# Performance work log

Hardware: AMD Instinct MI355X
Metric: run time of the kernel (lower is better)

## Reference

```python
import jax, jax.numpy as jnp
import numpy as np

DIM = 256; HEADS = 8; DK = 64; DV = 64; FH = 32; FW = 32; B = 16
INK = HEADS * DK; INV = HEADS * DV; N = FH * FW
SCALE = DK ** -0.5; EPS = 1e-5


def _pos_indices():
    pos = np.stack(np.meshgrid(np.arange(FH), np.arange(FW), indexing='ij'), axis=-1).reshape(-1, 2)
    rel = np.abs(pos[:, None, :] - pos[None, :, :])  # [N,N,2]
    return jnp.asarray(rel[..., 0] * FW + rel[..., 1], jnp.int32)  # [N,N]


def _bn(x, g, b, m, v):
    # eval-mode BatchNorm2d over channel axis 1
    s = (g / jnp.sqrt(v + EPS))
    return x * s[None, :, None, None] + (b - m * s)[None, :, None, None]


def setup_inputs() -> dict:
    key = jax.random.key(0)
    ks = jax.random.split(key, 24)
    f32 = jnp.float32
    def bn_params(k, c):
        k1, k2, k3, k4 = jax.random.split(k, 4)
        return (jax.random.normal(k1, (c,), f32) * 0.1 + 1.0,
                jax.random.normal(k2, (c,), f32) * 0.1,
                jax.random.normal(k3, (c,), f32) * 0.1,
                jax.random.uniform(k4, (c,), f32) + 0.5)
    gq, bq, mq, vq = bn_params(ks[1], INK)
    gk, bk, mk, vk = bn_params(ks[3], INK)
    gv, bv, mv, vv = bn_params(ks[5], INV)
    go, bo, mo, vo = bn_params(ks[7], DIM)
    return {
        'x': jax.random.normal(ks[0], (B, DIM, FH, FW), f32),
        'wq': jax.random.normal(ks[2], (INK, DIM), f32) * (DIM ** -0.5),
        'gq': gq, 'bq': bq, 'mq': mq, 'vq': vq,
        'wk': jax.random.normal(ks[4], (INK, DIM), f32) * (DIM ** -0.5),
        'gk': gk, 'bk': bk, 'mk': mk, 'vk': vk,
        'wv': jax.random.normal(ks[6], (INV, DIM), f32) * (DIM ** -0.5),
        'gv': gv, 'bv': bv, 'mv': mv, 'vv': vv,
        'emb': jax.random.normal(ks[8], (N, HEADS), f32) * 0.02,
        'w_out': jax.random.normal(ks[9], (DIM, INV), f32) * (INV ** -0.5),
        'b_out': jax.random.normal(ks[10], (DIM,), f32) * 0.02,
        'go': go, 'bo': bo, 'mo': mo, 'vo': vo,
        'pos_indices': _pos_indices(),
    }


def reference(x, wq, gq, bq, mq, vq, wk, gk, bk, mk, vk, wv, gv, bv, mv, vv,
              emb, w_out, b_out, go, bo, mo, vo, pos_indices):
    b = x.shape[0]
    # 1x1 conv == channel matmul
    q = _bn(jnp.einsum('bchw,oc->bohw', x, wq), gq, bq, mq, vq)
    k = _bn(jnp.einsum('bchw,oc->bohw', x, wk), gk, bk, mk, vk)
    v = _bn(jnp.einsum('bchw,oc->bohw', x, wv), gv, bv, mv, vv)
    # 'b (h d) x y -> b h (x y) d'
    def split_heads(t, d):
        return t.reshape(b, HEADS, d, N).transpose(0, 1, 3, 2)
    q = split_heads(q, DK); k = split_heads(k, DK); v = split_heads(v, DV)
    dots = jnp.einsum('bhid,bhjd->bhij', q, k) * SCALE  # [b,h,N,N]
    bias = emb[pos_indices]                               # [N,N,h] gather
    dots = dots + jnp.transpose(bias, (2, 0, 1))[None] / SCALE
    attn = jax.nn.softmax(dots, axis=-1)
    out = jnp.einsum('bhij,bhjd->bhid', attn, v)
    out = out.transpose(0, 1, 3, 2).reshape(b, INV, FH, FW)  # 'b h (x y) d -> b (h d) x y'
    hs = out * jnp.clip(out + 3.0, 0.0, 6.0) / 6.0           # Hardswish
    y = jnp.einsum('bchw,oc->bohw', hs, w_out) + b_out[None, :, None, None]
    return _bn(y, go, bo, mo, vo)
```

## Files before the change

kernel.cpp:

```cpp
#include <hip/hip_runtime.h>

typedef __attribute__((ext_vector_type(4))) float f32x4;
typedef __attribute__((ext_vector_type(8))) _Float16 f16x8;
typedef __attribute__((ext_vector_type(4))) _Float16 f16x4;

static __device__ __forceinline__ f32x4 mfma16f(f16x8 a, f16x8 b, f32x4 c) {
    return __builtin_amdgcn_mfma_f32_16x16x32_f16(a, b, c, 0, 0, 0);
}

__global__ __launch_bounds__(256) void prep(
    const float* __restrict__ x,
    const float* __restrict__ s0, const float* __restrict__ s1,
    const float* __restrict__ s2, const float* __restrict__ s3,
    _Float16* __restrict__ d0h, _Float16* __restrict__ d0l,
    _Float16* __restrict__ d1h, _Float16* __restrict__ d1l,
    _Float16* __restrict__ d2h, _Float16* __restrict__ d2l,
    _Float16* __restrict__ d3h, _Float16* __restrict__ d3l,
    _Float16* __restrict__ xth, _Float16* __restrict__ xtl)
{
    __shared__ float lt[32][36];
    const int t = threadIdx.x;
    const int bid = blockIdx.x;
    if (bid < 2048) {
        const int seg = bid >> 9;
        const int i = (bid & 511) * 256 + t;
        const float* src = (seg == 0) ? s0 : (seg == 1) ? s1 : (seg == 2) ? s2 : s3;
        _Float16* dh = (seg == 0) ? d0h : (seg == 1) ? d1h : (seg == 2) ? d2h : d3h;
        _Float16* dl = (seg == 0) ? d0l : (seg == 1) ? d1l : (seg == 2) ? d2l : d3l;
        const float f = src[i];
        const _Float16 h = (_Float16)f;
        dh[i] = h;
        dl[i] = (_Float16)(f - (float)h);
    } else {
        const int bid2 = bid - 2048;
        const int c0 = (bid2 & 7) * 32, hw0 = ((bid2 >> 3) & 31) * 32, b = bid2 >> 8;
        {
            const int cl = t >> 3, hw4 = (t & 7) * 4;
            *(f32x4*)&lt[cl][hw4] = *(const f32x4*)&x[((size_t)(b * 256 + c0 + cl)) * 1024 + hw0 + hw4];
        }
        __syncthreads();
        {
            const int hwl = t >> 3, c4 = (t & 7) * 4;
            f16x4 hv, lv;
#pragma unroll
            for (int e = 0; e < 4; ++e) {
                const float f = lt[c4 + e][hwl];
                const _Float16 h = (_Float16)f;
                hv[e] = h;
                lv[e] = (_Float16)(f - (float)h);
            }
            const size_t off = ((size_t)(b * 1024 + hw0 + hwl)) * 256 + c0 + c4;
            *(f16x4*)(xth + off) = hv;
            *(f16x4*)(xtl + off) = lv;
        }
    }
}

__global__ __launch_bounds__(256) void qkv_mfma(
    const _Float16* __restrict__ xth, const _Float16* __restrict__ xtl,
    const _Float16* __restrict__ wqh, const _Float16* __restrict__ wql,
    const _Float16* __restrict__ wkh, const _Float16* __restrict__ wkl,
    const _Float16* __restrict__ wvh, const _Float16* __restrict__ wvl,
    const float* __restrict__ gq, const float* __restrict__ bq, const float* __restrict__ mq, const float* __restrict__ vq,
    const float* __restrict__ gk, const float* __restrict__ bk, const float* __restrict__ mk, const float* __restrict__ vk,
    const float* __restrict__ gv, const float* __restrict__ bv, const float* __restrict__ mv, const float* __restrict__ vv,
    _Float16* __restrict__ qh, _Float16* __restrict__ ql,
    _Float16* __restrict__ kh,
    _Float16* __restrict__ vt)
{
    __shared__ _Float16 Ah[128][72];
    __shared__ _Float16 Al[128][72];
    __shared__ float sc_l[128], tc_l[128];

    const int t = threadIdx.x;
    const int bn = blockIdx.x;
    const int m0 = blockIdx.y * 128;
    const int proj = bn >> 2;
    const int o0 = (bn & 3) * 128;
    const int bimg = m0 >> 10;
    const int nb = m0 & 1023;

    const _Float16* Wh = (proj == 0) ? wqh : (proj == 1) ? wkh : wvh;
    const _Float16* Wl = (proj == 0) ? wql : (proj == 1) ? wkl : wvl;
    const float* G  = (proj == 0) ? gq : (proj == 1) ? gk : gv;
    const float* Bt = (proj == 0) ? bq : (proj == 1) ? bk : bv;
    const float* Mn = (proj == 0) ? mq : (proj == 1) ? mk : mv;
    const float* Vr = (proj == 0) ? vq : (proj == 1) ? vk : vv;

    if (t < 128) {
        const int o = o0 + t;
        float s = G[o] / sqrtf(Vr[o] + 1e-5f);
        float tt = Bt[o] - Mn[o] * s;
        if (proj == 0) { s *= 0.125f; tt *= 0.125f; }
        sc_l[t] = s; tc_l[t] = tt;
    }

    const int wave = t >> 6, lane = t & 63;
    const int quad = lane >> 4, l16 = lane & 15;
    const int wm = (wave >> 1) * 64, wn = (wave & 1) * 64;

    f32x4 acc[4][4] = {};

    for (int c0 = 0; c0 < 256; c0 += 64) {
        __syncthreads();
        {
            int r = t >> 3;
            const int cs = (t & 7) * 8;
#pragma unroll
            for (int p = 0; p < 4; ++p, r += 32) {
                const size_t off = ((size_t)(bimg * 1024 + nb + r)) * 256 + c0 + cs;
                *(f16x8*)&Ah[r][cs] = *(const f16x8*)(xth + off);
                *(f16x8*)&Al[r][cs] = *(const f16x8*)(xtl + off);
            }
        }
        __syncthreads();
#pragma unroll
        for (int kk = 0; kk < 2; ++kk) {
            f16x8 ah[4], al[4], bh[4], bl[4];
#pragma unroll
            for (int mi = 0; mi < 4; ++mi) {
                ah[mi] = *(const f16x8*)&Ah[wm + mi * 16 + l16][kk * 32 + quad * 8];
                al[mi] = *(const f16x8*)&Al[wm + mi * 16 + l16][kk * 32 + quad * 8];
            }
#pragma unroll
            for (int nj = 0; nj < 4; ++nj) {
                const size_t off = ((size_t)(o0 + wn + nj * 16 + l16)) * 256 + c0 + kk * 32 + quad * 8;
                bh[nj] = *(const f16x8*)(Wh + off);
                if (proj < 2) bl[nj] = *(const f16x8*)(Wl + off);
            }
            if (proj < 2) {
#pragma unroll
                for (int nj = 0; nj < 4; ++nj)
#pragma unroll
                    for (int mi = 0; mi < 4; ++mi) {
                        acc[nj][mi] = mfma16f(bh[nj], ah[mi], acc[nj][mi]);
                        acc[nj][mi] = mfma16f(bh[nj], al[mi], acc[nj][mi]);
                        acc[nj][mi] = mfma16f(bl[nj], ah[mi], acc[nj][mi]);
                    }
            } else {
#pragma unroll
                for (int mi = 0; mi < 4; ++mi)
#pragma unroll
                    for (int nj = 0; nj < 4; ++nj) {
                        acc[mi][nj] = mfma16f(ah[mi], bh[nj], acc[mi][nj]);
                        acc[mi][nj] = mfma16f(al[mi], bh[nj], acc[mi][nj]);
                    }
            }
        }
    }

    if (proj < 2) {
        _Float16* Oh = (proj == 0) ? qh : kh;
#pragma unroll
        for (int nj = 0; nj < 4; ++nj) {
            const int olb = wn + nj * 16 + quad * 4;
            const int ob = o0 + olb;
            const int head = ob >> 6, d0 = ob & 63;
#pragma unroll
            for (int mi = 0; mi < 4; ++mi) {
                const int n = nb + wm + mi * 16 + l16;
                f16x4 hv, lv;
#pragma unroll
                for (int rr = 0; rr < 4; ++rr) {
                    const float val = acc[nj][mi][rr] * sc_l[olb + rr] + tc_l[olb + rr];
                    const _Float16 h = (_Float16)val;
                    hv[rr] = h;
                    lv[rr] = (_Float16)(val - (float)h);
                }
                const size_t off = (((size_t)(bimg * 8 + head)) * 1024 + n) * 64 + d0;
                *(f16x4*)(Oh + off) = hv;
                if (proj == 0) *(f16x4*)(ql + off) = lv;
            }
        }
    } else {
#pragma unroll
        for (int nj = 0; nj < 4; ++nj) {
            const int olb = wn + nj * 16 + l16;
            const int o = o0 + olb;
            const int head = o >> 6, d = o & 63;
            const float s = sc_l[olb], tt = tc_l[olb];
#pragma unroll
            for (int mi = 0; mi < 4; ++mi) {
                const int n0 = nb + wm + mi * 16 + quad * 4;
                f16x4 v4;
#pragma unroll
                for (int rr = 0; rr < 4; ++rr) v4[rr] = (_Float16)(acc[mi][nj][rr] * s + tt);
                *(f16x4*)(vt + (((size_t)(bimg * 8 + head)) * 64 + d) * 1024 + n0) = v4;
            }
        }
    }
}

__global__ __launch_bounds__(512, 4) void attn_mfma(
    const _Float16* __restrict__ qh, const _Float16* __restrict__ ql,
    const _Float16* __restrict__ kh,
    const _Float16* __restrict__ vt,
    const float* __restrict__ emb,
    _Float16* __restrict__ hsh)
{
    __shared__ float    emb_s[1024];
    __shared__ _Float16 kth[64][76];
    __shared__ _Float16 vts[64][76];

    const int t = threadIdx.x;
    const int bid = blockIdx.x;
    const int bh = bid & 127, qb = bid >> 7;
    const int b = bh >> 3, h = bh & 7;
    const int wave = t >> 6, lane = t & 63;
    const int quad = lane >> 4, l16 = lane & 15;
    const int q0 = qb * 128 + wave * 16;
    const float L2E = 1.44269504f;

    for (int i = t; i < 1024; i += 512) emb_s[i] = (8.0f * emb[i * 8 + h] - 12.0f) * L2E;

    const size_t base = (size_t)bh * 65536;

    f16x8 qfh[2], qfl[2];
#pragma unroll
    for (int kk = 0; kk < 2; ++kk) {
        const size_t off = base + (size_t)(q0 + l16) * 64 + kk * 32 + quad * 8;
        qfh[kk] = *(const f16x8*)(qh + off);
        qfl[kk] = *(const f16x8*)(ql + off);
    }

    const int ig0 = q0 + l16;
    const int xi = ig0 >> 5, yi = ig0 & 31;

    const int sr = t >> 3;
    const int scs = (t & 7) * 8;

    f16x8 pkh, pvv;
    pkh = *(const f16x8*)(kh + base + (size_t)sr * 64 + scs);
    pvv = *(const f16x8*)(vt + base + (size_t)sr * 1024 + scs);

    f32x4 ao[4] = {};
    float lsum = 0.0f;

    for (int jb = 0; jb < 16; ++jb) {
        __syncthreads();
        *(f16x8*)&kth[sr][scs] = pkh;
        *(f16x8*)&vts[sr][scs] = pvv;
        __syncthreads();
        if (jb < 15) {
            pkh = *(const f16x8*)(kh + base + (size_t)((jb + 1) * 64 + sr) * 64 + scs);
            pvv = *(const f16x8*)(vt + base + (size_t)sr * 1024 + (jb + 1) * 64 + scs);
        }

#pragma unroll
        for (int nj = 0; nj < 4; ++nj) {
            const f16x8 kf0 = *(const f16x8*)&kth[nj * 16 + l16][quad * 8];
            const f16x8 kf1 = *(const f16x8*)&kth[nj * 16 + l16][32 + quad * 8];

            f32x4 ss = {};
            __builtin_amdgcn_s_setprio(1);
            ss = mfma16f(kf0, qfh[0], ss);
            ss = mfma16f(kf0, qfl[0], ss);
            ss = mfma16f(kf1, qfh[1], ss);
            ss = mfma16f(kf1, qfl[1], ss);
            __builtin_amdgcn_s_setprio(0);

            const int xj = 2 * jb + (nj >> 1);
            const int yj0 = ((nj & 1) << 4) + quad * 4;
            const int dxo = abs(xi - xj) << 5;
            const int yq = yi - yj0;
            const float p0 = __builtin_amdgcn_exp2f(fmaf(ss[0], L2E, emb_s[dxo + abs(yq)]));
            const float p1 = __builtin_amdgcn_exp2f(fmaf(ss[1], L2E, emb_s[dxo + abs(yq - 1)]));
            const float p2 = __builtin_amdgcn_exp2f(fmaf(ss[2], L2E, emb_s[dxo + abs(yq - 2)]));
            const float p3 = __builtin_amdgcn_exp2f(fmaf(ss[3], L2E, emb_s[dxo + abs(yq - 3)]));
            lsum += (p0 + p1) + (p2 + p3);
            f16x4 pa;
            pa[0] = (_Float16)p0; pa[1] = (_Float16)p1;
            pa[2] = (_Float16)p2; pa[3] = (_Float16)p3;

            f16x4 vf[4];
#pragma unroll
            for (int dj = 0; dj < 4; ++dj)
                vf[dj] = *(const f16x4*)&vts[dj * 16 + l16][nj * 16 + quad * 4];
            __builtin_amdgcn_s_setprio(1);
#pragma unroll
            for (int dj = 0; dj < 4; ++dj)
                ao[dj] = __builtin_amdgcn_mfma_f32_16x16x16f16(pa, vf[dj], ao[dj], 0, 0, 0);
            __builtin_amdgcn_s_setprio(0);
        }
    }

    float l = lsum;
    l += __shfl_xor(l, 16, 64);
    l += __shfl_xor(l, 32, 64);
    float inv[4];
#pragma unroll
    for (int r = 0; r < 4; ++r)
        inv[r] = 1.0f / __shfl(l, quad * 4 + r, 64);
#pragma unroll
    for (int r = 0; r < 4; ++r) {
        const int ig = q0 + quad * 4 + r;
#pragma unroll
        for (int dj = 0; dj < 4; ++dj) {
            const float o = ao[dj][r] * inv[r];
            const float hsw = o * fminf(fmaxf(o + 3.0f, 0.0f), 6.0f) * (1.0f / 6.0f);
            hsh[((size_t)(b * 1024 + ig)) * 512 + h * 64 + dj * 16 + l16] = (_Float16)hsw;
        }
    }
}

__global__ __launch_bounds__(256) void out_mfma(
    const _Float16* __restrict__ hsh,
    const _Float16* __restrict__ woh, const _Float16* __restrict__ wol,
    const float* __restrict__ b_out, const float* __restrict__ go, const float* __restrict__ bo,
    const float* __restrict__ mo, const float* __restrict__ vo, float* __restrict__ y)
{
    __shared__ _Float16 Ah[64][136];

    const int t = threadIdx.x;
    const int m0 = blockIdx.x * 64;
    const int o0 = blockIdx.y * 128;
    const int bimg = m0 >> 10, nb = m0 & 1023;
    const int wave = t >> 6, lane = t & 63;
    const int quad = lane >> 4, l16 = lane & 15;
    const int wm = (wave >> 1) * 32, wn = (wave & 1) * 64;

    f32x4 acc[2][4] = {};
    f16x8 bh[4], bl[4], nbh[4], nbl[4];

#pragma unroll
    for (int nj = 0; nj < 4; ++nj) {
        const size_t off = ((size_t)(o0 + wn + nj * 16 + l16)) * 512 + quad * 8;
        bh[nj] = *(const f16x8*)(woh + off);
        bl[nj] = *(const f16x8*)(wol + off);
    }

#pragma unroll
    for (int it = 0; it < 16; ++it) {
        const int c0 = (it >> 2) * 128, kk = it & 3;
        if (kk == 0) {
            __syncthreads();
            const int cs = (t & 7) * 16;
#pragma unroll
            for (int p = 0; p < 2; ++p) {
                const int r = (t >> 3) + p * 32;
                *(f16x8*)&Ah[r][cs]     = *(const f16x8*)(hsh + ((size_t)(m0 + r)) * 512 + c0 + cs);
                *(f16x8*)&Ah[r][cs + 8] = *(const f16x8*)(hsh + ((size_t)(m0 + r)) * 512 + c0 + cs + 8);
            }
            __syncthreads();
        }
        if (it < 15) {
            const int nit = it + 1;
            const int nc0 = (nit >> 2) * 128, nkk = nit & 3;
#pragma unroll
            for (int nj = 0; nj < 4; ++nj) {
                const size_t off = ((size_t)(o0 + wn + nj * 16 + l16)) * 512 + nc0 + nkk * 32 + quad * 8;
                nbh[nj] = *(const f16x8*)(woh + off);
                nbl[nj] = *(const f16x8*)(wol + off);
            }
        }
        f16x8 ah[2];
#pragma unroll
        for (int mi = 0; mi < 2; ++mi)
            ah[mi] = *(const f16x8*)&Ah[wm + mi * 16 + l16][kk * 32 + quad * 8];
#pragma unroll
        for (int mi = 0; mi < 2; ++mi)
#pragma unroll
            for (int nj = 0; nj < 4; ++nj) {
                acc[mi][nj] = mfma16f(ah[mi], bh[nj], acc[mi][nj]);
                acc[mi][nj] = mfma16f(ah[mi], bl[nj], acc[mi][nj]);
            }
#pragma unroll
        for (int nj = 0; nj < 4; ++nj) { bh[nj] = nbh[nj]; bl[nj] = nbl[nj]; }
    }

#pragma unroll
    for (int nj = 0; nj < 4; ++nj) {
        const int o = o0 + wn + nj * 16 + l16;
        const float s = go[o] / sqrtf(vo[o] + 1e-5f);
        const float tt = bo[o] - mo[o] * s;
        const float bf = b_out[o];
#pragma unroll
        for (int mi = 0; mi < 2; ++mi) {
            const int hw = nb + wm + mi * 16 + quad * 4;
            f32x4 v4;
#pragma unroll
            for (int rr = 0; rr < 4; ++rr) v4[rr] = (acc[mi][nj][rr] + bf) * s + tt;
            *(f32x4*)&y[((size_t)(bimg * 256 + o)) * 1024 + hw] = v4;
        }
    }
}

extern "C" void kernel_launch(void* const* d_in, const int* in_sizes, int n_in,
                              void* d_out, int out_size, void* d_ws, size_t ws_size,
                              hipStream_t stream) {
    const float* x     = (const float*)d_in[0];
    const float* wq    = (const float*)d_in[1];
    const float* gq    = (const float*)d_in[2];
    const float* bq    = (const float*)d_in[3];
    const float* mq    = (const float*)d_in[4];
    const float* vq    = (const float*)d_in[5];
    const float* wk    = (const float*)d_in[6];
    const float* gk    = (const float*)d_in[7];
    const float* bk    = (const float*)d_in[8];
    const float* mk    = (const float*)d_in[9];
    const float* vk    = (const float*)d_in[10];
    const float* wv    = (const float*)d_in[11];
    const float* gv    = (const float*)d_in[12];
    const float* bv    = (const float*)d_in[13];
    const float* mv    = (const float*)d_in[14];
    const float* vv    = (const float*)d_in[15];
    const float* emb   = (const float*)d_in[16];
    const float* w_out = (const float*)d_in[17];
    const float* b_out = (const float*)d_in[18];
    const float* go    = (const float*)d_in[19];
    const float* bo    = (const float*)d_in[20];
    const float* mo    = (const float*)d_in[21];
    const float* vo    = (const float*)d_in[22];

    _Float16* us = (_Float16*)d_ws;
    _Float16* xth = us;
    _Float16* xtl = us + 4194304;
    _Float16* hsh = us;
    _Float16* wsp = us + 16777216;
    _Float16* wqh = wsp,            *wql = wsp + 131072;
    _Float16* wkh = wsp + 262144,   *wkl = wsp + 393216;
    _Float16* wvh = wsp + 524288,   *wvl = wsp + 655360;
    _Float16* woh = wsp + 786432,   *wol = wsp + 917504;
    _Float16* qv  = us + 17825792;
    _Float16* qhw = qv,             *qlw = qv + 8388608;
    _Float16* khw = qv + 16777216;
    _Float16* vtw = qv + 33554432;

    prep<<<6144, 256, 0, stream>>>(x, wq, wk, wv, w_out,
                                   wqh, wql, wkh, wkl, wvh, wvl, woh, wol,
                                   xth, xtl);

    qkv_mfma<<<dim3(12, 128), 256, 0, stream>>>(
        xth, xtl, wqh, wql, wkh, wkl, wvh, wvl,
        gq, bq, mq, vq, gk, bk, mk, vk, gv, bv, mv, vv,
        qhw, qlw, khw, vtw);

    attn_mfma<<<1024, 512, 0, stream>>>(
        qhw, qlw, khw, vtw, emb, hsh);

    out_mfma<<<dim3(256, 2), 256, 0, stream>>>(
        hsh, woh, wol, b_out, go, bo, mo, vo, (float*)d_out);
}
```

Before: 282.5 us.

## Use direct global-to-LDS loads with XOR swizzle and narrower QKV output tiles

The QKV projection kernel now stages the x tiles through global_load_lds (direct DMA into LDS) instead of loading into registers and then storing to shared memory. The padded LDS layout is replaced by an XOR-swizzled one to avoid bank conflicts. The output-channel tile drops from 128 to 64, which doubles the grid and halves the accumulators, and launch bounds now ask for 4 blocks per CU to raise occupancy. In exchange, x tiles are reloaded twice as often across blocks, and the swizzle has to match between the DMA writes and the MFMA reads.

```diff
diff --git a/kernel.cpp b/kernel.cpp
--- a/kernel.cpp
+++ b/kernel.cpp
@@ -56,7 +56,7 @@
     }
 }
 
-__global__ __launch_bounds__(256) void qkv_mfma(
+__global__ __launch_bounds__(256, 4) void qkv_mfma(
     const _Float16* __restrict__ xth, const _Float16* __restrict__ xtl,
     const _Float16* __restrict__ wqh, const _Float16* __restrict__ wql,
     const _Float16* __restrict__ wkh, const _Float16* __restrict__ wkl,
@@ -68,15 +68,15 @@
     _Float16* __restrict__ kh,
     _Float16* __restrict__ vt)
 {
-    __shared__ _Float16 Ah[128][72];
-    __shared__ _Float16 Al[128][72];
-    __shared__ float sc_l[128], tc_l[128];
+    __shared__ _Float16 Ah[128][64];
+    __shared__ _Float16 Al[128][64];
+    __shared__ float sc_l[64], tc_l[64];
 
     const int t = threadIdx.x;
     const int bn = blockIdx.x;
     const int m0 = blockIdx.y * 128;
-    const int proj = bn >> 2;
-    const int o0 = (bn & 3) * 128;
+    const int proj = bn >> 3;
+    const int o0 = (bn & 7) * 64;
     const int bimg = m0 >> 10;
     const int nb = m0 & 1023;
 
@@ -87,7 +87,7 @@
     const float* Mn = (proj == 0) ? mq : (proj == 1) ? mk : mv;
     const float* Vr = (proj == 0) ? vq : (proj == 1) ? vk : vv;
 
-    if (t < 128) {
+    if (t < 64) {
         const int o = o0 + t;
         float s = G[o] / sqrtf(Vr[o] + 1e-5f);
         float tt = Bt[o] - Mn[o] * s;
@@ -97,62 +97,76 @@
 
     const int wave = t >> 6, lane = t & 63;
     const int quad = lane >> 4, l16 = lane & 15;
-    const int wm = (wave >> 1) * 64, wn = (wave & 1) * 64;
-
-    f32x4 acc[4][4] = {};
+    const int wm = (wave >> 1) * 64;
+    const int wn = (wave & 1) * 32;
+
+    const int srow = wave * 32;
+    const int lr8 = lane >> 3;
+    const int lsl = lane & 7;
+
+    f32x4 acc[8] = {};
 
     for (int c0 = 0; c0 < 256; c0 += 64) {
+#pragma unroll
+        for (int p = 0; p < 4; ++p) {
+            const int r = srow + p * 8 + lr8;
+            const int sg = lsl ^ (r & 7);
+            const size_t goff = ((size_t)(bimg * 1024 + nb + r)) * 256 + c0 + sg * 8;
+            __builtin_amdgcn_global_load_lds(
+                (const __attribute__((address_space(1))) void*)(xth + goff),
+                (__attribute__((address_space(3))) void*)&Ah[srow + p * 8][0], 16, 0, 0);
+            __builtin_amdgcn_global_load_lds(
+                (const __attribute__((address_space(1))) void*)(xtl + goff),
+                (__attribute__((address_space(3))) void*)&Al[srow + p * 8][0], 16, 0, 0);
+        }
         __syncthreads();
-        {
-            int r = t >> 3;
-            const int cs = (t & 7) * 8;
-#pragma unroll
-            for (int p = 0; p < 4; ++p, r += 32) {
-                const size_t off = ((size_t)(bimg * 1024 + nb + r)) * 256 + c0 + cs;
-                *(f16x8*)&Ah[r][cs] = *(const f16x8*)(xth + off);
-                *(f16x8*)&Al[r][cs] = *(const f16x8*)(xtl + off);
-            }
-        }
-        __syncthreads();
+
 #pragma unroll
         for (int kk = 0; kk < 2; ++kk) {
-            f16x8 ah[4], al[4], bh[4], bl[4];
-#pragma unroll
-            for (int mi = 0; mi < 4; ++mi) {
-                ah[mi] = *(const f16x8*)&Ah[wm + mi * 16 + l16][kk * 32 + quad * 8];
-                al[mi] = *(const f16x8*)&Al[wm + mi * 16 + l16][kk * 32 + quad * 8];
-            }
-#pragma unroll
-            for (int nj = 0; nj < 4; ++nj) {
+            f16x8 ah[4], al[4], bh[2], bl[2];
+#pragma unroll
+            for (int nj = 0; nj < 2; ++nj) {
                 const size_t off = ((size_t)(o0 + wn + nj * 16 + l16)) * 256 + c0 + kk * 32 + quad * 8;
                 bh[nj] = *(const f16x8*)(Wh + off);
                 if (proj < 2) bl[nj] = *(const f16x8*)(Wl + off);
             }
+#pragma unroll
+            for (int mi = 0; mi < 4; ++mi) {
+                const int arow = wm + mi * 16 + l16;
+                const int sl = ((kk * 4 + quad) ^ (arow & 7)) * 8;
+                ah[mi] = *(const f16x8*)&Ah[arow][sl];
+                al[mi] = *(const f16x8*)&Al[arow][sl];
+            }
             if (proj < 2) {
 #pragma unroll
-                for (int nj = 0; nj < 4; ++nj)
+                for (int nj = 0; nj < 2; ++nj)
 #pragma unroll
                     for (int mi = 0; mi < 4; ++mi) {
-                        acc[nj][mi] = mfma16f(bh[nj], ah[mi], acc[nj][mi]);
-                        acc[nj][mi] = mfma16f(bh[nj], al[mi], acc[nj][mi]);
-                        acc[nj][mi] = mfma16f(bl[nj], ah[mi], acc[nj][mi]);
+                        f32x4 a = acc[nj * 4 + mi];
+                        a = mfma16f(bh[nj], ah[mi], a);
+                        a = mfma16f(bh[nj], al[mi], a);
+                        a = mfma16f(bl[nj], ah[mi], a);
+                        acc[nj * 4 + mi] = a;
                     }
             } else {
 #pragma unroll
                 for (int mi = 0; mi < 4; ++mi)
 #pragma unroll
-                    for (int nj = 0; nj < 4; ++nj) {
-                        acc[mi][nj] = mfma16f(ah[mi], bh[nj], acc[mi][nj]);
-                        acc[mi][nj] = mfma16f(al[mi], bh[nj], acc[mi][nj]);
+                    for (int nj = 0; nj < 2; ++nj) {
+                        f32x4 a = acc[mi * 2 + nj];
+                        a = mfma16f(ah[mi], bh[nj], a);
+                        a = mfma16f(al[mi], bh[nj], a);
+                        acc[mi * 2 + nj] = a;
                     }
             }
         }
+        __syncthreads();
     }
 
     if (proj < 2) {
         _Float16* Oh = (proj == 0) ? qh : kh;
 #pragma unroll
-        for (int nj = 0; nj < 4; ++nj) {
+        for (int nj = 0; nj < 2; ++nj) {
             const int olb = wn + nj * 16 + quad * 4;
             const int ob = o0 + olb;
             const int head = ob >> 6, d0 = ob & 63;
@@ -162,7 +176,7 @@
                 f16x4 hv, lv;
 #pragma unroll
                 for (int rr = 0; rr < 4; ++rr) {
-                    const float val = acc[nj][mi][rr] * sc_l[olb + rr] + tc_l[olb + rr];
+                    const float val = acc[nj * 4 + mi][rr] * sc_l[olb + rr] + tc_l[olb + rr];
                     const _Float16 h = (_Float16)val;
                     hv[rr] = h;
                     lv[rr] = (_Float16)(val - (float)h);
@@ -174,7 +188,7 @@
         }
     } else {
 #pragma unroll
-        for (int nj = 0; nj < 4; ++nj) {
+        for (int nj = 0; nj < 2; ++nj) {
             const int olb = wn + nj * 16 + l16;
             const int o = o0 + olb;
             const int head = o >> 6, d = o & 63;
@@ -184,7 +198,7 @@
                 const int n0 = nb + wm + mi * 16 + quad * 4;
                 f16x4 v4;
 #pragma unroll
-                for (int rr = 0; rr < 4; ++rr) v4[rr] = (_Float16)(acc[mi][nj][rr] * s + tt);
+                for (int rr = 0; rr < 4; ++rr) v4[rr] = (_Float16)(acc[mi * 2 + nj][rr] * s + tt);
                 *(f16x4*)(vt + (((size_t)(bimg * 8 + head)) * 64 + d) * 1024 + n0) = v4;
             }
         }
@@ -430,7 +444,7 @@
                                    wqh, wql, wkh, wkl, wvh, wvl, woh, wol,
                                    xth, xtl);
 
-    qkv_mfma<<<dim3(12, 128), 256, 0, stream>>>(
+    qkv_mfma<<<dim3(24, 128), 256, 0, stream>>>(
         xth, xtl, wqh, wql, wkh, wkl, wvh, wvl,
         gq, bq, mq, vq, gk, bk, mk, vk, gv, bv, mv, vv,
         qhw, qlw, khw, vtw);
```

Result: slower. 327.8 us (+16.0%).
